# Optimization experiments

Hardware: AMD Instinct MI355X
Metric: run time of the kernel (lower is better)

## Reference

```python
import jax, jax.numpy as jnp
import numpy as np

# ---- static config (matches init_kwargs) ----
B, N_CAMS, C, H, W = 2, 6, 256, 32, 88
BEV_H = BEV_W = 100
NQ = BEV_H * BEV_W
D_PILLAR = 4
HEADS = 8
LEVELS = 3
HEAD_DIM = C // HEADS
PC_RANGE = (-51.2, -51.2, -5.0, 51.2, 51.2, 3.0)
OGFH, OGFW = 256, 704


def _make_lidar2img():
    """Plausible lidar->image projection matrices (K @ [R|t]) for 6 ring cameras."""
    mats = np.zeros((B, N_CAMS, 4, 4), np.float32)
    K = np.array([[557.0, 0.0, OGFW / 2.0], [0.0, 557.0, OGFH / 2.0], [0.0, 0.0, 1.0]], np.float64)
    for b in range(B):
        for n in range(N_CAMS):
            yaw = 2.0 * np.pi * n / N_CAMS + 0.05 * b
            fwd = np.array([np.cos(yaw), np.sin(yaw), 0.0])
            right = np.array([np.sin(yaw), -np.cos(yaw), 0.0])
            down = np.array([0.0, 0.0, -1.0])
            R = np.stack([right, down, fwd])  # lidar -> camera axes
            cam_center = np.array([1.5 * np.cos(yaw), 1.5 * np.sin(yaw), 1.8])
            t = -R @ cam_center
            P = K @ np.concatenate([R, t[:, None]], axis=1)
            mats[b, n, :3, :] = P.astype(np.float32)
            mats[b, n, 3, 3] = 1.0
    return jnp.asarray(mats)


def setup_inputs() -> dict:
    key = jax.random.key(0)
    ks = jax.random.split(key, 16)
    s = 0.02
    return {
        'imgs': jax.random.normal(ks[0], (B, N_CAMS, C, H, W), jnp.float32),
        'lidar2img': _make_lidar2img(),
        'bev_query': jax.random.normal(ks[1], (NQ, 1, C), jnp.float32) * s,
        'bev_pos': jax.random.normal(ks[2], (1, NQ, C), jnp.float32) * s,
        'cams_embeds': jax.random.normal(ks[3], (N_CAMS, C), jnp.float32) * s,
        'level_embeds': jax.random.normal(ks[4], (LEVELS, C), jnp.float32) * s,
        'w_fpn': jax.random.normal(ks[5], (LEVELS, C, C), jnp.float32) * s,
        'b_fpn': jnp.zeros((LEVELS, C), jnp.float32),
        'w_value': jax.random.normal(ks[6], (C, C), jnp.float32) * s,
        'b_value': jnp.zeros((C,), jnp.float32),
        'w_off': jax.random.normal(ks[7], (C, HEADS * LEVELS * D_PILLAR * 2), jnp.float32) * s,
        'b_off': jax.random.normal(ks[8], (HEADS * LEVELS * D_PILLAR * 2,), jnp.float32) * 0.5,
        'w_attn': jax.random.normal(ks[9], (C, HEADS * LEVELS * D_PILLAR), jnp.float32) * s,
        'b_attn': jnp.zeros((HEADS * LEVELS * D_PILLAR,), jnp.float32),
        'w_out': jax.random.normal(ks[10], (C, C), jnp.float32) * s,
        'b_out': jnp.zeros((C,), jnp.float32),
        'w_ts1': jax.random.normal(ks[11], (C, C), jnp.float32) * s,
        'b_ts1': jnp.zeros((C,), jnp.float32),
        'w_ts2': jax.random.normal(ks[12], (C, C), jnp.float32) * s,
        'b_ts2': jnp.zeros((C,), jnp.float32),
    }


def _deform_sample(v, loc, h, w):
    """Bilinear sample (grid_sample, zero padding, align_corners=False).
    v: [N, heads, h*w, dh]; loc: [N, heads, Q, 2] normalized to [0,1]. -> [N, heads, Q, dh]"""
    x = loc[..., 0] * w - 0.5
    y = loc[..., 1] * h - 0.5
    x0 = jnp.floor(x)
    y0 = jnp.floor(y)
    out = jnp.zeros(v.shape[:2] + (loc.shape[2], v.shape[-1]), v.dtype)
    for dx in (0, 1):
        for dy in (0, 1):
            xi = x0 + dx
            yi = y0 + dy
            wgt = (1.0 - jnp.abs(x - xi)) * (1.0 - jnp.abs(y - yi))
            valid = (xi >= 0) & (xi < w) & (yi >= 0) & (yi < h)
            idx = (jnp.clip(yi, 0, h - 1) * w + jnp.clip(xi, 0, w - 1)).astype(jnp.int32)
            g = jnp.take_along_axis(v, idx[..., None], axis=2)
            out = out + g * (wgt * valid)[..., None]
    return out


def _forward(imgs, lidar2img, bev_query, bev_pos, cams_embeds, level_embeds,
             w_fpn, b_fpn, w_value, b_value, w_off, b_off, w_attn, b_attn,
             w_out, b_out, w_ts1, b_ts1, w_ts2, b_ts2):
    # ---- FPN: 3 levels at strides 1/2/4 with per-level 1x1 projection ----
    x = imgs.reshape(B * N_CAMS, C, H, W)
    feats, shapes = [], []
    cur = x
    for l in range(LEVELS):
        if l > 0:
            bn, c, h, w = cur.shape
            cur = cur.reshape(bn, c, h // 2, 2, w // 2, 2).mean(axis=(3, 5))
        f = jnp.einsum('bchw,cd->bdhw', cur, w_fpn[l]) + b_fpn[l][None, :, None, None]
        feats.append(f)
        shapes.append((f.shape[2], f.shape[3]))
    # ---- flatten levels + cam/level embeds: [N, sum_hw, B, C] ----
    flat = []
    for l, f in enumerate(feats):
        h, w = shapes[l]
        fl = jnp.transpose(f.reshape(B, N_CAMS, C, h * w), (1, 0, 3, 2))  # [N,B,hw,C]
        fl = fl + cams_embeds[:, None, None, :] + level_embeds[l][None, None, None, :]
        flat.append(fl)
    feat_flatten = jnp.transpose(jnp.concatenate(flat, axis=2), (0, 2, 1, 3))  # [N,sum_hw,B,C]

    # ---- 3D pillar reference points, normalized [0,1] ----
    zrange = PC_RANGE[5] - PC_RANGE[2]
    zs = jnp.linspace(0.5, zrange - 0.5, D_PILLAR) / zrange
    xs = (jnp.arange(BEV_W, dtype=jnp.float32) + 0.5) / BEV_W
    ys = (jnp.arange(BEV_H, dtype=jnp.float32) + 0.5) / BEV_H
    gy, gx = jnp.meshgrid(ys, xs, indexing='ij')
    ref2d = jnp.stack([gx.ravel(), gy.ravel()], axis=-1)  # [NQ,2]
    ref3d = jnp.concatenate([
        jnp.broadcast_to(ref2d[None], (D_PILLAR, NQ, 2)),
        jnp.broadcast_to(zs[:, None, None].astype(jnp.float32), (D_PILLAR, NQ, 1)),
    ], axis=-1)
    scale = jnp.array([PC_RANGE[3] - PC_RANGE[0], PC_RANGE[4] - PC_RANGE[1], zrange], jnp.float32)
    shift = jnp.array(PC_RANGE[:3], jnp.float32)
    xyz = ref3d * scale + shift
    homog = jnp.concatenate([xyz, jnp.ones((D_PILLAR, NQ, 1), jnp.float32)], axis=-1)

    # ---- point sampling: project to each camera, mask invalid pixels ----
    pts = jnp.einsum('bnij,dqj->nbqdi', lidar2img, homog)  # [N,B,NQ,D,4]
    eps = 1e-5
    depth = pts[..., 2]
    xy = pts[..., :2] / jnp.maximum(depth[..., None], eps)
    ref_cam = xy / jnp.array([OGFW, OGFH], jnp.float32)  # [N,B,NQ,D,2]
    bev_mask = ((depth > eps) & (ref_cam[..., 0] > 0) & (ref_cam[..., 0] < 1)
                & (ref_cam[..., 1] > 0) & (ref_cam[..., 1] < 1))  # [N,B,NQ,D]

    pos = bev_pos[0]  # [NQ,C]

    def sca(query, value, ref_b, mask_b):
        # query [NQ,C]; value [N,sum_hw,C]; ref_b [N,NQ,D,2]; mask_b [N,NQ,D]
        residual = query
        q = query + pos
        v = value @ w_value + b_value
        off = (q @ w_off + b_off).reshape(NQ, HEADS, LEVELS, D_PILLAR, 2)
        attn = jax.nn.softmax((q @ w_attn + b_attn).reshape(NQ, HEADS, LEVELS * D_PILLAR), axis=-1)
        attn = attn.reshape(NQ, HEADS, LEVELS, D_PILLAR)
        out = jnp.zeros((N_CAMS, NQ, HEADS, HEAD_DIM), q.dtype)
        start = 0
        for l, (h, w) in enumerate(shapes):
            hw = h * w
            v_l = jnp.transpose(v[:, start:start + hw].reshape(N_CAMS, hw, HEADS, HEAD_DIM), (0, 2, 1, 3))
            start += hw
            norm = jnp.array([w, h], q.dtype)
            loc = ref_b[:, :, None, :, :] + off[None, :, :, l] / norm  # [N,NQ,heads,D,2]
            loc = jnp.transpose(loc, (0, 2, 1, 3, 4)).reshape(N_CAMS, HEADS, NQ * D_PILLAR, 2)
            s = _deform_sample(v_l, loc, h, w).reshape(N_CAMS, HEADS, NQ, D_PILLAR, HEAD_DIM)
            out = out + jnp.einsum('nhqpd,qhp->nqhd', s, attn[:, :, l])
        out = out.reshape(N_CAMS, NQ, C)
        valid = mask_b.any(axis=-1)  # [N,NQ]
        slots = (out * valid[..., None].astype(out.dtype)).sum(axis=0)
        count = jnp.maximum(valid.sum(axis=0), 1).astype(out.dtype)[:, None]
        slots = slots / count
        return slots @ w_out + b_out + residual

    def tsblock(t):
        return jax.nn.relu(t @ w_ts1 + b_ts1) @ w_ts2 + b_ts2

    bq = jnp.transpose(bev_query, (1, 0, 2))[0]  # [NQ,C]
    groups = []
    ego = bq
    for b in range(B):
        val = feat_flatten[:, :, b, :]
        r = ref_cam[:, b]
        m = bev_mask[:, b]
        if b == 0:
            for _ in range(2):
                bq = tsblock(sca(bq, val, r, m))
            ego = bq
            groups.append(ego.reshape(C, BEV_W, BEV_H))
        else:
            nb = tsblock(sca(ego, val, r, m))
            groups.append(nb.reshape(C, BEV_W, BEV_H))
    bev_groups = jnp.stack(groups, axis=0)  # [B,C,BEV_W,BEV_H]
    return bq[None], bev_groups


def reference(imgs, lidar2img, bev_query, bev_pos, cams_embeds, level_embeds,
              w_fpn, b_fpn, w_value, b_value, w_off, b_off, w_attn, b_attn,
              w_out, b_out, w_ts1, b_ts1, w_ts2, b_ts2):
    return _forward(imgs, lidar2img, bev_query, bev_pos, cams_embeds, level_embeds,
                    w_fpn, b_fpn, w_value, b_value, w_off, b_off, w_attn, b_attn,
                    w_out, b_out, w_ts1, b_ts1, w_ts2, b_ts2)
```

## Files before the change

kernel.cpp:

```cpp
#include <hip/hip_runtime.h>
#include <math.h>

typedef __attribute__((ext_vector_type(8))) short bf16x8;
typedef __attribute__((ext_vector_type(4))) float f32x4;

__device__ __forceinline__ unsigned short f2bf(float x) {
  union { float f; unsigned int u; } v; v.f = x;
  unsigned int r = v.u + 0x7fffu + ((v.u >> 16) & 1u);
  return (unsigned short)(r >> 16);
}
__device__ __forceinline__ float bf2f(unsigned short b) {
  union { unsigned int u; float f; } v; v.u = ((unsigned int)b) << 16; return v.f;
}
__device__ __forceinline__ void split2(float x, unsigned short& h, unsigned short& l) {
  h = f2bf(x);
  l = f2bf(x - bf2f(h));
}
__device__ __forceinline__ int fsi(int q, int c) { return q * 256 + (c ^ ((q & 7) << 2)); }

__device__ __forceinline__ void writeP(unsigned short* __restrict__ P, int col, int k,
                                       unsigned short h, unsigned short l) {
  int tile = col >> 4;
  int lane = (((k >> 3) & 3) << 4) | (col & 15);
  int ks = k >> 5, j8 = k & 7;
  size_t base = ((size_t)(tile >> 1) * 16384) + (size_t)(((tile & 1) << 4) + ks * 2) * 512
              + (size_t)lane * 8 + j8;
  P[base] = h;
  P[base + 512] = l;
}

__device__ __forceinline__ void ld16(const unsigned short* b, bf16x8* f) {
  const unsigned short* b1 = b + 2048;
  const unsigned short* b2 = b + 4096;
  const unsigned short* b3 = b + 6144;
  asm volatile(
    "global_load_dwordx4 %0, %16, off\n\t"
    "global_load_dwordx4 %1, %16, off offset:1024\n\t"
    "global_load_dwordx4 %2, %16, off offset:2048\n\t"
    "global_load_dwordx4 %3, %16, off offset:3072\n\t"
    "global_load_dwordx4 %4, %17, off\n\t"
    "global_load_dwordx4 %5, %17, off offset:1024\n\t"
    "global_load_dwordx4 %6, %17, off offset:2048\n\t"
    "global_load_dwordx4 %7, %17, off offset:3072\n\t"
    "global_load_dwordx4 %8, %18, off\n\t"
    "global_load_dwordx4 %9, %18, off offset:1024\n\t"
    "global_load_dwordx4 %10, %18, off offset:2048\n\t"
    "global_load_dwordx4 %11, %18, off offset:3072\n\t"
    "global_load_dwordx4 %12, %19, off\n\t"
    "global_load_dwordx4 %13, %19, off offset:1024\n\t"
    "global_load_dwordx4 %14, %19, off offset:2048\n\t"
    "global_load_dwordx4 %15, %19, off offset:3072\n\t"
    "s_waitcnt vmcnt(0)"
    : "=&v"(f[0]), "=&v"(f[1]), "=&v"(f[2]), "=&v"(f[3]),
      "=&v"(f[4]), "=&v"(f[5]), "=&v"(f[6]), "=&v"(f[7]),
      "=&v"(f[8]), "=&v"(f[9]), "=&v"(f[10]), "=&v"(f[11]),
      "=&v"(f[12]), "=&v"(f[13]), "=&v"(f[14]), "=&v"(f[15])
    : "v"(b), "v"(b1), "v"(b2), "v"(b3));
}

__device__ __forceinline__ void ld16nw(const unsigned short* b, bf16x8* f) {
  const unsigned short* b1 = b + 2048;
  const unsigned short* b2 = b + 4096;
  const unsigned short* b3 = b + 6144;
  asm volatile(
    "global_load_dwordx4 %0, %16, off\n\t"
    "global_load_dwordx4 %1, %16, off offset:1024\n\t"
    "global_load_dwordx4 %2, %16, off offset:2048\n\t"
    "global_load_dwordx4 %3, %16, off offset:3072\n\t"
    "global_load_dwordx4 %4, %17, off\n\t"
    "global_load_dwordx4 %5, %17, off offset:1024\n\t"
    "global_load_dwordx4 %6, %17, off offset:2048\n\t"
    "global_load_dwordx4 %7, %17, off offset:3072\n\t"
    "global_load_dwordx4 %8, %18, off\n\t"
    "global_load_dwordx4 %9, %18, off offset:1024\n\t"
    "global_load_dwordx4 %10, %18, off offset:2048\n\t"
    "global_load_dwordx4 %11, %18, off offset:3072\n\t"
    "global_load_dwordx4 %12, %19, off\n\t"
    "global_load_dwordx4 %13, %19, off offset:1024\n\t"
    "global_load_dwordx4 %14, %19, off offset:2048\n\t"
    "global_load_dwordx4 %15, %19, off offset:3072"
    : "=&v"(f[0]), "=&v"(f[1]), "=&v"(f[2]), "=&v"(f[3]),
      "=&v"(f[4]), "=&v"(f[5]), "=&v"(f[6]), "=&v"(f[7]),
      "=&v"(f[8]), "=&v"(f[9]), "=&v"(f[10]), "=&v"(f[11]),
      "=&v"(f[12]), "=&v"(f[13]), "=&v"(f[14]), "=&v"(f[15])
    : "v"(b), "v"(b1), "v"(b2), "v"(b3));
}

#define MFMA(a, b, c) __builtin_amdgcn_mfma_f32_16x16x32_bf16(a, b, c, 0, 0, 0)

__device__ __forceinline__ void gemm2t32(
    const unsigned short* __restrict__ Wp, int tile0,
    int lane, int lk, int l15,
    const unsigned short (&AS)[2][32][32][8], f32x4 (&acc)[2][2])
{
  const unsigned short* base = Wp + ((size_t)(tile0 >> 1) * 16384) + (size_t)lane * 8;
  bf16x8 f[32];
  ld16nw(base, f);
  ld16(base + 8192, f + 16);
  __builtin_amdgcn_sched_barrier(0);
#pragma unroll
  for (int ks = 0; ks < 8; ++ks) {
    bf16x8 h0 = f[2 * ks], l0 = f[2 * ks + 1];
    bf16x8 h1 = f[16 + 2 * ks], l1 = f[17 + 2 * ks];
#pragma unroll
    for (int nf = 0; nf < 2; ++nf) {
      bf16x8 bqh = *(const bf16x8*)&AS[0][ks * 4 + lk][nf * 16 + l15][0];
      bf16x8 bql = *(const bf16x8*)&AS[1][ks * 4 + lk][nf * 16 + l15][0];
      acc[0][nf] = MFMA(h0, bqh, acc[0][nf]);
      acc[0][nf] = MFMA(h0, bql, acc[0][nf]);
      acc[0][nf] = MFMA(l0, bqh, acc[0][nf]);
      acc[1][nf] = MFMA(h1, bqh, acc[1][nf]);
      acc[1][nf] = MFMA(h1, bql, acc[1][nf]);
      acc[1][nf] = MFMA(l1, bqh, acc[1][nf]);
    }
  }
}

__device__ __forceinline__ void gemm2t64(
    const unsigned short* __restrict__ Wp, int tile0,
    int lane, int lk, int l15,
    const unsigned short (&AS)[2][32][64][8], f32x4 (&acc)[2][4])
{
  const unsigned short* base = Wp + ((size_t)(tile0 >> 1) * 16384) + (size_t)lane * 8;
  bf16x8 f[32];
  ld16nw(base, f);
  ld16(base + 8192, f + 16);
  __builtin_amdgcn_sched_barrier(0);
#pragma unroll
  for (int ks = 0; ks < 8; ++ks) {
    bf16x8 h0 = f[2 * ks], l0 = f[2 * ks + 1];
    bf16x8 h1 = f[16 + 2 * ks], l1 = f[17 + 2 * ks];
#pragma unroll
    for (int nf = 0; nf < 4; ++nf) {
      bf16x8 bqh = *(const bf16x8*)&AS[0][ks * 4 + lk][nf * 16 + l15][0];
      bf16x8 bql = *(const bf16x8*)&AS[1][ks * 4 + lk][nf * 16 + l15][0];
      acc[0][nf] = MFMA(h0, bqh, acc[0][nf]);
      acc[0][nf] = MFMA(h0, bql, acc[0][nf]);
      acc[0][nf] = MFMA(l0, bqh, acc[0][nf]);
      acc[1][nf] = MFMA(h1, bqh, acc[1][nf]);
      acc[1][nf] = MFMA(h1, bql, acc[1][nf]);
      acc[1][nf] = MFMA(l1, bqh, acc[1][nf]);
    }
  }
}

__device__ __forceinline__ void gemm1t64(
    const unsigned short* __restrict__ Wp, int tile,
    int lane, int lk, int l15,
    const unsigned short (&AS)[2][32][64][8], f32x4 (&acc)[4])
{
  const unsigned short* base = Wp + ((size_t)(tile >> 1) * 16384) + (size_t)(tile & 1) * 8192 + (size_t)lane * 8;
  bf16x8 f[16];
  ld16(base, f);
  __builtin_amdgcn_sched_barrier(0);
#pragma unroll
  for (int ks = 0; ks < 8; ++ks) {
    bf16x8 eh = f[2 * ks], el = f[2 * ks + 1];
#pragma unroll
    for (int nf = 0; nf < 4; ++nf) {
      bf16x8 bqh = *(const bf16x8*)&AS[0][ks * 4 + lk][nf * 16 + l15][0];
      bf16x8 bql = *(const bf16x8*)&AS[1][ks * 4 + lk][nf * 16 + l15][0];
      acc[nf] = MFMA(eh, bqh, acc[nf]);
      acc[nf] = MFMA(eh, bql, acc[nf]);
      acc[nf] = MFMA(el, bqh, acc[nf]);
    }
  }
}

__global__ __launch_bounds__(256) void pool2x2(const float* __restrict__ in, float* __restrict__ out,
                                               int h, int w, int total)
{
  int i = blockIdx.x * 256 + threadIdx.x;
  if (i >= total) return;
  int x = i % w; int r = i / w; int y = r % h; int ci = r / h;
  const float* p = in + (size_t)ci * (4 * h * w) + (size_t)(2 * y) * (2 * w) + 2 * x;
  out[i] = (p[0] + p[1] + p[2 * w] + p[2 * w + 1]) * 0.25f;
}

__global__ __launch_bounds__(256) void prep(
    const float* __restrict__ wo, const float* __restrict__ bo,
    const float* __restrict__ wa, const float* __restrict__ ba,
    const float* __restrict__ wout, const float* __restrict__ wts1, const float* __restrict__ wts2,
    const float* __restrict__ wfpn, const float* __restrict__ wval,
    const float* __restrict__ cams, const float* __restrict__ lev,
    const float* __restrict__ bfpn, const float* __restrict__ bval,
    unsigned short* __restrict__ wcatP, float* __restrict__ bcat,
    unsigned short* __restrict__ woutP, unsigned short* __restrict__ wts1P,
    unsigned short* __restrict__ w45P, unsigned short* __restrict__ wcombP,
    float* __restrict__ e2)
{
  int bb = blockIdx.x, t = threadIdx.x;
  if (bb < 768) {
    int l = bb >> 8, i = bb & 255, j = t;
    const float* a = wfpn + ((size_t)l * 256 + i) * 256;
    float acc = 0.f;
    for (int k = 0; k < 256; ++k) acc = fmaf(a[k], wval[(size_t)k * 256 + j], acc);
    unsigned short h, lo; split2(acc, h, lo);
    writeP(wcombP, l * 256 + j, i, h, lo);
  } else if (bb < 1056) {
    int i = (bb - 768) * 256 + t;
    int c = i >> 8, k = i & 255;
    float v = (c < 192) ? wo[k * 192 + c] : wa[k * 96 + (c - 192)];
    unsigned short h, l; split2(v, h, l);
    writeP(wcatP, c, k, h, l);
    if (i < 288) bcat[i] = (i < 192) ? bo[i] : ba[i - 192];
  } else if (bb < 1312) {
    int i = (bb - 1056) * 256 + t;
    int nn = i >> 8, k = i & 255;
    float v = wout[(size_t)k * 256 + nn];
    unsigned short h, l; split2(v, h, l);
    writeP(woutP, nn, k, h, l);
  } else if (bb < 1568) {
    int i = (bb - 1312) * 256 + t;
    int nn = i >> 8, k = i & 255;
    float v = wts1[(size_t)k * 256 + nn];
    unsigned short h, l; split2(v, h, l);
    writeP(wts1P, nn, k, h, l);
  } else if (bb < 1824) {
    int i = (bb - 1568) * 256 + t;
    int nn = i >> 8, k = i & 255;
    float v = wts2[(size_t)k * 256 + nn];
    unsigned short h, l; split2(v, h, l);
    writeP(w45P, nn, k, h, l);
  } else if (bb < 2112) {
    int mp = bb - 1824;
    int k = t;
    float acc = 0.f;
    for (int j = 0; j < 256; ++j) {
      float wc = (mp < 192) ? wo[j * 192 + mp] : wa[j * 96 + (mp - 192)];
      acc = fmaf(wts2[(size_t)k * 256 + j], wc, acc);
    }
    unsigned short h, l; split2(acc, h, l);
    writeP(w45P, 256 + mp, k, h, l);
  } else {
    int e = bb - 2112;
    int n = e / 3, l = e % 3, j = t;
    float acc = bval[j];
    for (int k = 0; k < 256; ++k) {
      float s = cams[n * 256 + k] + lev[l * 256 + k] + bfpn[l * 256 + k];
      acc = fmaf(s, wval[(size_t)k * 256 + j], acc);
    }
    e2[(size_t)e * 256 + j] = acc;
  }
}

__global__ __launch_bounds__(512) void value_fused(
    const float* __restrict__ imgs, const float* __restrict__ cur1a, const float* __restrict__ cur2a,
    const unsigned short* __restrict__ wcombP,
    const float* __restrict__ e2, float* __restrict__ Vall)
{
  __shared__ __align__(16) unsigned short AS[2][32][32][8];
  int t = threadIdx.x, wid = t >> 6, lane = t & 63, l15 = lane & 15, lk = lane >> 4;
  int bx = blockIdx.x, cam = blockIdx.y, bz = blockIdx.z;
  const float* img0 = imgs + (size_t)bz * 4325376;
  const float* cur1 = cur1a + (size_t)bz * 1081344;
  const float* cur2 = cur2a + (size_t)bz * 270336;
  float* V = Vall + (size_t)bz * 5677056;
  int level, tb, hw; const float* src;
  if (bx < 88)       { level = 0; tb = bx;       hw = 2816; src = img0; }
  else if (bx < 110) { level = 1; tb = bx - 88;  hw = 704;  src = cur1; }
  else               { level = 2; tb = bx - 110; hw = 176;  src = cur2; }
  int p0 = tb * 32;
  const int LST[3] = {0, 2816, 3520};
  src += (size_t)cam * 256 * hw;

  {
    int pos = t & 31, kg = t >> 5;
    bool ok = (p0 + pos) < hw;
    const float* col = src + p0 + pos;
    float vals[16];
#pragma unroll
    for (int i = 0; i < 16; ++i) {
      int k = kg * 16 + i;
      vals[i] = ok ? col[(size_t)k * hw] : 0.f;
    }
#pragma unroll
    for (int half = 0; half < 2; ++half) {
      int ch = kg * 2 + half;
      bf16x8 hv, lv;
#pragma unroll
      for (int j = 0; j < 8; ++j) {
        unsigned short h, l; split2(vals[half * 8 + j], h, l);
        hv[j] = (short)h; lv[j] = (short)l;
      }
      *(bf16x8*)&AS[0][ch][pos][0] = hv;
      *(bf16x8*)&AS[1][ch][pos][0] = lv;
    }
  }
  __syncthreads();

  f32x4 zed = {0.f, 0.f, 0.f, 0.f};
  f32x4 acc[2][2] = {{zed, zed}, {zed, zed}};
  gemm2t32(wcombP, level * 16 + wid * 2, lane, lk, l15, AS, acc);
  __syncthreads();

  float* ASf = (float*)(&AS[0][0][0][0]);
  const float* bias = e2 + (size_t)(cam * 3 + level) * 256;
#pragma unroll
  for (int mf = 0; mf < 2; ++mf) {
    int chb = (wid * 2 + mf) * 16 + lk * 4;
    float4 b4 = *(const float4*)(bias + chb);
#pragma unroll
    for (int nf = 0; nf < 2; ++nf) {
      int q = nf * 16 + l15;
      float4 o;
      o.x = acc[mf][nf][0] + b4.x; o.y = acc[mf][nf][1] + b4.y;
      o.z = acc[mf][nf][2] + b4.z; o.w = acc[mf][nf][3] + b4.w;
      *(float4*)&ASf[fsi(q, chb)] = o;
    }
  }
  __syncthreads();
  float* Vb = V + ((size_t)cam * 3696 + LST[level] + p0) * 256;
#pragma unroll
  for (int j = 0; j < 4; ++j) {
    int g = t + j * 512;
    int q = g >> 6, c = (g & 63) * 4;
    if (p0 + q < hw)
      *(float4*)(Vb + (size_t)q * 256 + c) = *(const float4*)&ASf[fsi(q, c)];
  }
}

__global__ __launch_bounds__(512) void init_fused(
    const float* __restrict__ bev_pos, const float* __restrict__ bev_query,
    const float* __restrict__ bts2,
    const unsigned short* __restrict__ wcatP, const float* __restrict__ bcat,
    float* __restrict__ posA, float* __restrict__ posB,
    float* __restrict__ qtmpA, float* __restrict__ qtmpB)
{
  __shared__ __align__(16) unsigned short AS[2][32][64][8];
  float* ASf = (float*)(&AS[0][0][0][0]);
  int t = threadIdx.x, wid = t >> 6, lane = t & 63, l15 = lane & 15, lk = lane >> 4;
  int r0 = blockIdx.x * 64;
  int y = blockIdx.y;
  const float* base = y ? bev_query : bev_pos;
  const float* padd = y ? bev_pos : nullptr;
  const float* rb = y ? nullptr : bts2;
  float* oA = y ? qtmpA : posA;
  float* oB = y ? qtmpB : posB;
  f32x4 zed = {0.f, 0.f, 0.f, 0.f};

#pragma unroll
  for (int j = 0; j < 8; ++j) {
    int g = t + j * 512;
    int q = g >> 6, c = (g & 63) * 4;
    int rq = r0 + q; if (rq > 9999) rq = 9999;
    float4 a = *(const float4*)(base + (size_t)rq * 256 + c);
    if (padd) {
      float4 p = *(const float4*)(padd + (size_t)rq * 256 + c);
      a.x += p.x; a.y += p.y; a.z += p.z; a.w += p.w;
    }
    if (rb) {
      float4 rv = *(const float4*)(rb + c);
      a.x += rv.x; a.y += rv.y; a.z += rv.z; a.w += rv.w;
    }
    ushort4 hh, ll;
    split2(a.x, hh.x, ll.x); split2(a.y, hh.y, ll.y);
    split2(a.z, hh.z, ll.z); split2(a.w, hh.w, ll.w);
    *(ushort4*)&AS[0][c >> 3][q][c & 7] = hh;
    *(ushort4*)&AS[1][c >> 3][q][c & 7] = ll;
  }
  __syncthreads();

  f32x4 acc[2][4] = {{zed, zed, zed, zed}, {zed, zed, zed, zed}};
  gemm2t64(wcatP, wid * 2, lane, lk, l15, AS, acc);
  f32x4 acc3[4] = {zed, zed, zed, zed};
  if (wid < 2) gemm1t64(wcatP, 16 + wid, lane, lk, l15, AS, acc3);
  __syncthreads();
#pragma unroll
  for (int mf = 0; mf < 2; ++mf) {
    int chb = (wid * 2 + mf) * 16 + lk * 4;
    float4 b4 = *(const float4*)(bcat + chb);
#pragma unroll
    for (int nf = 0; nf < 4; ++nf) {
      int q = nf * 16 + l15;
      float4 o;
      o.x = acc[mf][nf][0] + b4.x; o.y = acc[mf][nf][1] + b4.y;
      o.z = acc[mf][nf][2] + b4.z; o.w = acc[mf][nf][3] + b4.w;
      *(float4*)&ASf[fsi(q, chb)] = o;
    }
  }
  if (wid < 2) {
    int ce = wid * 16 + lk * 4;
    float4 b4 = *(const float4*)(bcat + 256 + ce);
#pragma unroll
    for (int nf = 0; nf < 4; ++nf) {
      int qg = r0 + nf * 16 + l15;
      if (qg < 10000) {
        float4 o;
        o.x = acc3[nf][0] + b4.x; o.y = acc3[nf][1] + b4.y;
        o.z = acc3[nf][2] + b4.z; o.w = acc3[nf][3] + b4.w;
        *(float4*)(oB + (size_t)qg * 32 + ce) = o;
      }
    }
  }
  __syncthreads();
#pragma unroll
  for (int j = 0; j < 8; ++j) {
    int g = t + j * 512;
    int q = g >> 6, c = (g & 63) * 4;
    int qg = r0 + q;
    if (qg < 10000)
      *(float4*)(oA + (size_t)qg * 256 + c) = *(const float4*)&ASf[fsi(q, c)];
  }
}

__global__ __launch_bounds__(512) void fused_iter(
    const float* __restrict__ slots, const float* __restrict__ qin,
    const unsigned short* __restrict__ woutP, const unsigned short* __restrict__ wts1P,
    const unsigned short* __restrict__ w45P,
    const float* __restrict__ bout, const float* __restrict__ bts1,
    const float* __restrict__ bts2,
    float* __restrict__ qout, float* __restrict__ outA, float* __restrict__ outB,
    float* __restrict__ qtmpA, float* __restrict__ qtmpB)
{
  __shared__ __align__(16) unsigned short AS[2][32][64][8];
  float* ASf = (float*)(&AS[0][0][0][0]);
  int t = threadIdx.x, wid = t >> 6, lane = t & 63, l15 = lane & 15, lk = lane >> 4;
  int r0 = blockIdx.x * 64;
  f32x4 zed = {0.f, 0.f, 0.f, 0.f};

#pragma unroll
  for (int j = 0; j < 8; ++j) {
    int g = t + j * 512;
    int q = g >> 6, c = (g & 63) * 4;
    int rq = r0 + q; if (rq > 9999) rq = 9999;
    float4 a = *(const float4*)(slots + (size_t)rq * 256 + c);
    ushort4 hh, ll;
    split2(a.x, hh.x, ll.x); split2(a.y, hh.y, ll.y);
    split2(a.z, hh.z, ll.z); split2(a.w, hh.w, ll.w);
    *(ushort4*)&AS[0][c >> 3][q][c & 7] = hh;
    *(ushort4*)&AS[1][c >> 3][q][c & 7] = ll;
  }
  __syncthreads();

  {
    f32x4 acc[2][4] = {{zed, zed, zed, zed}, {zed, zed, zed, zed}};
    gemm2t64(woutP, wid * 2, lane, lk, l15, AS, acc);
    __syncthreads();
    float4 qreg[8];
#pragma unroll
    for (int j = 0; j < 8; ++j) {
      int g = t + j * 512;
      int q = g >> 6, c = (g & 63) * 4;
      int rq = r0 + q; if (rq > 9999) rq = 9999;
      qreg[j] = *(const float4*)(qin + (size_t)rq * 256 + c);
    }
#pragma unroll
    for (int j = 0; j < 8; ++j) {
      int g = t + j * 512;
      int q = g >> 6, c = (g & 63) * 4;
      *(float4*)&ASf[fsi(q, c)] = qreg[j];
    }
    __syncthreads();
    float4 rr[2][4];
#pragma unroll
    for (int mf = 0; mf < 2; ++mf) {
      int chb = (wid * 2 + mf) * 16 + lk * 4;
#pragma unroll
      for (int nf = 0; nf < 4; ++nf)
        rr[mf][nf] = *(const float4*)&ASf[fsi(nf * 16 + l15, chb)];
    }
    __syncthreads();
#pragma unroll
    for (int mf = 0; mf < 2; ++mf) {
      int chb = (wid * 2 + mf) * 16 + lk * 4;
      float4 b4 = *(const float4*)(bout + chb);
#pragma unroll
      for (int nf = 0; nf < 4; ++nf) {
        int q = nf * 16 + l15;
        float v0 = acc[mf][nf][0] + b4.x + rr[mf][nf].x;
        float v1 = acc[mf][nf][1] + b4.y + rr[mf][nf].y;
        float v2 = acc[mf][nf][2] + b4.z + rr[mf][nf].z;
        float v3 = acc[mf][nf][3] + b4.w + rr[mf][nf].w;
        ushort4 hh, ll;
        split2(v0, hh.x, ll.x); split2(v1, hh.y, ll.y);
        split2(v2, hh.z, ll.z); split2(v3, hh.w, ll.w);
        *(ushort4*)&AS[0][chb >> 3][q][chb & 7] = hh;
        *(ushort4*)&AS[1][chb >> 3][q][chb & 7] = ll;
      }
    }
    __syncthreads();
  }
  {
    f32x4 acc[2][4] = {{zed, zed, zed, zed}, {zed, zed, zed, zed}};
    gemm2t64(wts1P, wid * 2, lane, lk, l15, AS, acc);
    __syncthreads();
#pragma unroll
    for (int mf = 0; mf < 2; ++mf) {
      int chb = (wid * 2 + mf) * 16 + lk * 4;
      float4 b4 = *(const float4*)(bts1 + chb);
#pragma unroll
      for (int nf = 0; nf < 4; ++nf) {
        int q = nf * 16 + l15;
        float v0 = fmaxf(acc[mf][nf][0] + b4.x, 0.f);
        float v1 = fmaxf(acc[mf][nf][1] + b4.y, 0.f);
        float v2 = fmaxf(acc[mf][nf][2] + b4.z, 0.f);
        float v3 = fmaxf(acc[mf][nf][3] + b4.w, 0.f);
        ushort4 hh, ll;
        split2(v0, hh.x, ll.x); split2(v1, hh.y, ll.y);
        split2(v2, hh.z, ll.z); split2(v3, hh.w, ll.w);
        *(ushort4*)&AS[0][chb >> 3][q][chb & 7] = hh;
        *(ushort4*)&AS[1][chb >> 3][q][chb & 7] = ll;
      }
    }
    __syncthreads();
  }
  {
    f32x4 accA[2][4] = {{zed, zed, zed, zed}, {zed, zed, zed, zed}};
    f32x4 accB[2][4] = {{zed, zed, zed, zed}, {zed, zed, zed, zed}};
    if (wid < 4 || qtmpA) {
      gemm2t64(w45P, wid * 4,     lane, lk, l15, AS, accA);
      gemm2t64(w45P, wid * 4 + 2, lane, lk, l15, AS, accB);
    }
    f32x4 acc3[4] = {zed, zed, zed, zed};
    if (qtmpA && wid < 2) gemm1t64(w45P, 32 + wid, lane, lk, l15, AS, acc3);
    __syncthreads();
    if (wid < 4) {
#pragma unroll
      for (int half = 0; half < 2; ++half) {
#pragma unroll
        for (int mf = 0; mf < 2; ++mf) {
          int chb = (wid * 4 + half * 2 + mf) * 16 + lk * 4;
          float4 b4 = *(const float4*)(bts2 + chb);
#pragma unroll
          for (int nf = 0; nf < 4; ++nf) {
            int q = nf * 16 + l15;
            f32x4 a = half ? accB[mf][nf] : accA[mf][nf];
            float4 o;
            o.x = a[0] + b4.x; o.y = a[1] + b4.y;
            o.z = a[2] + b4.z; o.w = a[3] + b4.w;
            *(float4*)&ASf[fsi(q, chb)] = o;
          }
        }
      }
    }
    if (qtmpA && wid < 2) {
      int ce = wid * 16 + lk * 4;
#pragma unroll
      for (int nf = 0; nf < 4; ++nf) {
        int qg = r0 + nf * 16 + l15;
        if (qg < 10000) {
          float4 o;
          o.x = acc3[nf][0]; o.y = acc3[nf][1]; o.z = acc3[nf][2]; o.w = acc3[nf][3];
          *(float4*)(qtmpB + (size_t)qg * 32 + ce) = o;
        }
      }
    }
    __syncthreads();
#pragma unroll
    for (int j = 0; j < 8; ++j) {
      int g = t + j * 512;
      int q = g >> 6, c = (g & 63) * 4;
      int qg = r0 + q;
      if (qg < 10000) {
        float4 vq = *(const float4*)&ASf[fsi(q, c)];
        size_t go = (size_t)qg * 256 + c;
        *(float4*)(qout + go) = vq;
        if (outA) { *(float4*)(outA + go) = vq; *(float4*)(outB + go) = vq; }
      }
    }
    if (!qtmpA) return;
    __syncthreads();
    if (wid >= 4) {
#pragma unroll
      for (int half = 0; half < 2; ++half) {
#pragma unroll
        for (int mf = 0; mf < 2; ++mf) {
          int cc = ((wid - 4) * 4 + half * 2 + mf) * 16 + lk * 4;
#pragma unroll
          for (int nf = 0; nf < 4; ++nf) {
            int q = nf * 16 + l15;
            f32x4 a = half ? accB[mf][nf] : accA[mf][nf];
            float4 o;
            o.x = a[0]; o.y = a[1]; o.z = a[2]; o.w = a[3];
            *(float4*)&ASf[fsi(q, cc)] = o;
          }
        }
      }
    }
    __syncthreads();
#pragma unroll
    for (int j = 0; j < 8; ++j) {
      int g = t + j * 512;
      int q = g >> 6, c = (g & 63) * 4;
      int qg = r0 + q;
      if (qg < 10000)
        *(float4*)(qtmpA + (size_t)qg * 256 + c) = *(const float4*)&ASf[fsi(q, c)];
    }
  }
}

__global__ __launch_bounds__(256) void sca_sample(const float* __restrict__ qtmpA, const float* __restrict__ qtmpB,
                                                  const float* __restrict__ posA, const float* __restrict__ posB,
                                                  const float* __restrict__ V,
                                                  const float* __restrict__ l2i, float* __restrict__ slots)
{
  int b = blockIdx.x;
  int q = (b & 7) * 1250 + (b >> 3);
  int t = threadIdx.x;
  int head = t >> 5;
  __shared__ float raw[288];
  __shared__ float attnS[96];
  __shared__ float refx[6][4], refy[6][4];
  __shared__ int mnd[24];
  __shared__ int validn[6];
  __shared__ __align__(16) float w4[576][4];
  __shared__ __align__(16) int o4[576][4];

  {
    float x = qtmpA[(size_t)q * 256 + t];
    if (posA) x += posA[(size_t)q * 256 + t];
    raw[t] = x;
    if (t < 32) {
      float y = qtmpB[(size_t)q * 32 + t];
      if (posB) y += posB[(size_t)q * 32 + t];
      raw[256 + t] = y;
    }
  }
  if (t >= 32 && t < 56) {
    int tt = t - 32;
    int n = tt >> 2, d = tt & 3;
    const float* Mrow = l2i + n * 16;
    int qx = q % 100, qy = q / 100;
    float X = ((qx + 0.5f) / 100.0f) * 102.4f + (-51.2f);
    float Y = ((qy + 0.5f) / 100.0f) * 102.4f + (-51.2f);
    float zi = (d == 3) ? 7.5f : (0.5f + (float)d * (7.0f / 3.0f));
    float Z = zi + (-5.0f);
    float px = Mrow[0] * X + Mrow[1] * Y + Mrow[2] * Z + Mrow[3];
    float py = Mrow[4] * X + Mrow[5] * Y + Mrow[6] * Z + Mrow[7];
    float pz = Mrow[8] * X + Mrow[9] * Y + Mrow[10] * Z + Mrow[11];
    float dz = fmaxf(pz, 1e-5f);
    float xc = (px / dz) / 704.0f;
    float yc = (py / dz) / 256.0f;
    refx[n][d] = xc; refy[n][d] = yc;
    mnd[n * 4 + d] = (pz > 1e-5f) && (xc > 0.f) && (xc < 1.f) && (yc > 0.f) && (yc < 1.f);
  }
  __syncthreads();
  if (t < 8) {
    float mx = raw[192 + t * 12];
    for (int p = 1; p < 12; ++p) mx = fmaxf(mx, raw[192 + t * 12 + p]);
    float s = 0.f;
    float e[12];
#pragma unroll
    for (int p = 0; p < 12; ++p) { e[p] = __expf(raw[192 + t * 12 + p] - mx); s += e[p]; }
    float inv = 1.f / s;
#pragma unroll
    for (int p = 0; p < 12; ++p) attnS[t * 12 + p] = e[p] * inv;
  } else if (t < 14) {
    int n = t - 8;
    validn[n] = mnd[n * 4] | mnd[n * 4 + 1] | mnd[n * 4 + 2] | mnd[n * 4 + 3];
  }
  __syncthreads();

  int packed = 0, nv = 0;
#pragma unroll
  for (int n = 0; n < 6; ++n)
    if (validn[n]) { packed |= n << (3 * nv); nv++; }
  float invc = 1.f / (float)(nv > 1 ? nv : 1);

  const float WWf[3] = {88.f, 44.f, 22.f}, HHf[3] = {32.f, 16.f, 8.f};
  const int WWi[3] = {88, 44, 22}, STi[3] = {0, 2816, 3520};
  int npts = nv * 96;
  for (int pt = t; pt < npts; pt += 256) {
    int hd = pt & 7;
    int g = pt >> 3;
    int j = g % 12, ni = g / 12;
    int n = (packed >> (3 * ni)) & 7;
    int l = j >> 2, d = j & 3;
    float wwf = WWf[l], hhf = HHf[l];
    int wwi = WWi[l], st = STi[l];
    float a = attnS[hd * 12 + j] * invc;
    float ox = raw[hd * 24 + l * 8 + d * 2 + 0];
    float oy = raw[hd * 24 + l * 8 + d * 2 + 1];
    float x = refx[n][d] * wwf + ox - 0.5f;
    float y = refy[n][d] * hhf + oy - 0.5f;
    float x0 = floorf(x), y0 = floorf(y);
    float fx = x - x0, fy = y - y0;
    float wx0 = 1.f - fx, wy0 = 1.f - fy;
    float vx0 = (x0 >= 0.f && x0 < wwf) ? 1.f : 0.f;
    float vx1 = (x0 + 1.f >= 0.f && x0 + 1.f < wwf) ? 1.f : 0.f;
    float vy0 = (y0 >= 0.f && y0 < hhf) ? 1.f : 0.f;
    float vy1 = (y0 + 1.f >= 0.f && y0 + 1.f < hhf) ? 1.f : 0.f;
    w4[pt][0] = a * wx0 * wy0 * vx0 * vy0;
    w4[pt][1] = a * fx * wy0 * vx1 * vy0;
    w4[pt][2] = a * wx0 * fy * vx0 * vy1;
    w4[pt][3] = a * fx * fy * vx1 * vy1;
    int ix0 = (int)fminf(fmaxf(x0, 0.f), wwf - 1.f);
    int ix1 = (int)fminf(fmaxf(x0 + 1.f, 0.f), wwf - 1.f);
    int iy0 = (int)fminf(fmaxf(y0, 0.f), hhf - 1.f);
    int iy1 = (int)fminf(fmaxf(y0 + 1.f, 0.f), hhf - 1.f);
    int rA = (st + iy0 * wwi) << 10, rB = (st + iy1 * wwi) << 10;
    o4[pt][0] = rA + (ix0 << 10);
    o4[pt][1] = rA + (ix1 << 10);
    o4[pt][2] = rB + (ix0 << 10);
    o4[pt][3] = rB + (ix1 << 10);
  }
  __syncthreads();

  int t4 = t << 2;
  float acc0 = 0.f, acc1 = 0.f;
  int sl = 0;
#pragma unroll
  for (int n = 0; n < 6; ++n) {
    if (!validn[n]) continue;
    const char* Vn = (const char*)(V + (size_t)n * 946176);
    int pb = sl * 96 + head;
    sl++;
    float va[48];
#pragma unroll
    for (int j = 0; j < 12; ++j) {
      int4 o = *reinterpret_cast<const int4*>(&o4[pb + j * 8][0]);
      va[4 * j + 0] = *(const float*)(Vn + (unsigned)(o.x + t4));
      va[4 * j + 1] = *(const float*)(Vn + (unsigned)(o.y + t4));
      va[4 * j + 2] = *(const float*)(Vn + (unsigned)(o.z + t4));
      va[4 * j + 3] = *(const float*)(Vn + (unsigned)(o.w + t4));
    }
#pragma unroll
    for (int j = 0; j < 12; ++j) {
      float4 w = *reinterpret_cast<const float4*>(&w4[pb + j * 8][0]);
      acc0 = fmaf(w.x, va[4 * j + 0], acc0);
      acc1 = fmaf(w.y, va[4 * j + 1], acc1);
      acc0 = fmaf(w.z, va[4 * j + 2], acc0);
      acc1 = fmaf(w.w, va[4 * j + 3], acc1);
    }
  }
  slots[(size_t)q * 256 + t] = acc0 + acc1;
}

extern "C" void kernel_launch(void* const* d_in, const int* in_sizes, int n_in,
                              void* d_out, int out_size, void* d_ws, size_t ws_size,
                              hipStream_t stream)
{
  const float* imgs = (const float*)d_in[0];
  const float* l2i = (const float*)d_in[1];
  const float* bev_query = (const float*)d_in[2];
  const float* bev_pos = (const float*)d_in[3];
  const float* cams = (const float*)d_in[4];
  const float* lev = (const float*)d_in[5];
  const float* wfpn = (const float*)d_in[6];
  const float* bfpn = (const float*)d_in[7];
  const float* wval = (const float*)d_in[8];
  const float* bval = (const float*)d_in[9];
  const float* woff = (const float*)d_in[10];
  const float* boff = (const float*)d_in[11];
  const float* wattn = (const float*)d_in[12];
  const float* battn = (const float*)d_in[13];
  const float* wout = (const float*)d_in[14];
  const float* bout = (const float*)d_in[15];
  const float* wts1 = (const float*)d_in[16];
  const float* bts1 = (const float*)d_in[17];
  const float* wts2 = (const float*)d_in[18];
  const float* bts2 = (const float*)d_in[19];

  float* W = (float*)d_ws;
  size_t off = 0;
  auto alloc = [&](size_t n) { float* p = W + off; off += n; return p; };
  float* v    = alloc((size_t)2 * 5677056);
  float* cur1 = alloc((size_t)12 * 256 * 16 * 44);
  float* cur2 = alloc((size_t)12 * 256 * 8 * 22);
  float* bqA  = alloc(2560000);
  float* bqB  = alloc(2560000);
  float* qtmpA = alloc(2560000);
  float* qtmpB = alloc(320000);
  float* posA = alloc(2560000);
  float* posB = alloc(320000);
  float* slots = alloc(2560000);
  float* wcombPR = alloc(196608);
  float* wcatPR = alloc(73728);
  float* woutPR = alloc(65536);
  float* wts1PR = alloc(65536);
  float* w45PR = alloc(139264);
  float* bcat = alloc(512);
  float* e2 = alloc(4608);
  (void)ws_size; (void)in_sizes; (void)n_in; (void)out_size;

  unsigned short* wcombP = (unsigned short*)wcombPR;
  unsigned short* wcatP = (unsigned short*)wcatPR;
  unsigned short* woutP = (unsigned short*)woutPR;
  unsigned short* wts1P = (unsigned short*)wts1PR;
  unsigned short* w45P = (unsigned short*)w45PR;

  float* v0 = v;
  float* v1 = v + 5677056;
  float* OUT = (float*)d_out;

  pool2x2<<<8448, 256, 0, stream>>>(imgs, cur1, 16, 44, 2162688);
  pool2x2<<<2112, 256, 0, stream>>>(cur1, cur2, 8, 22, 540672);
  prep<<<2130, 256, 0, stream>>>(woff, boff, wattn, battn, wout, wts1, wts2, wfpn, wval,
                                 cams, lev, bfpn, bval,
                                 wcatP, bcat, woutP, wts1P, w45P, wcombP, e2);

  init_fused<<<dim3(157, 2), 512, 0, stream>>>(bev_pos, bev_query, bts2, wcatP, bcat,
                                               posA, posB, qtmpA, qtmpB);

  value_fused<<<dim3(116, 6, 2), 512, 0, stream>>>(imgs, cur1, cur2, wcombP, e2, v);

  sca_sample<<<10000, 256, 0, stream>>>(qtmpA, qtmpB, nullptr, nullptr, v0, l2i, slots);
  fused_iter<<<157, 512, 0, stream>>>(slots, bev_query,
      woutP, wts1P, w45P, bout, bts1, bts2,
      bqA, nullptr, nullptr, qtmpA, qtmpB);
  sca_sample<<<10000, 256, 0, stream>>>(qtmpA, qtmpB, posA, posB, v0, l2i, slots);
  fused_iter<<<157, 512, 0, stream>>>(slots, bqA,
      woutP, wts1P, w45P, bout, bts1, bts2,
      bqB, OUT, OUT + 2560000, qtmpA, qtmpB);
  sca_sample<<<10000, 256, 0, stream>>>(qtmpA, qtmpB, posA, posB, v1, l2i + 96, slots);
  fused_iter<<<157, 512, 0, stream>>>(slots, bqB,
      woutP, wts1P, w45P, bout, bts1, bts2,
      OUT + 5120000, nullptr, nullptr, nullptr, nullptr);
}
```

Before: 283.1 us.

## Merge pooling with prep and value projection with init into combined launches

The first 2x2 pooling is folded into the weight-prep kernel as extra blocks, and the value projection and BEV query init GEMMs are merged into one launch using blockIdx.z to pick the role. The value projection tile grows from 32 to 64 positions per block so it can reuse the 64-wide GEMM path, halving its block count. This removes two kernel launches and lets independent work run at the same time, at the cost of more registers per thread (32 loaded values) and some idle blocks in the third z-slice.

```diff
diff --git a/kernel.cpp b/kernel.cpp
--- a/kernel.cpp
+++ b/kernel.cpp
@@ -88,34 +88,6 @@
 
 #define MFMA(a, b, c) __builtin_amdgcn_mfma_f32_16x16x32_bf16(a, b, c, 0, 0, 0)
 
-__device__ __forceinline__ void gemm2t32(
-    const unsigned short* __restrict__ Wp, int tile0,
-    int lane, int lk, int l15,
-    const unsigned short (&AS)[2][32][32][8], f32x4 (&acc)[2][2])
-{
-  const unsigned short* base = Wp + ((size_t)(tile0 >> 1) * 16384) + (size_t)lane * 8;
-  bf16x8 f[32];
-  ld16nw(base, f);
-  ld16(base + 8192, f + 16);
-  __builtin_amdgcn_sched_barrier(0);
-#pragma unroll
-  for (int ks = 0; ks < 8; ++ks) {
-    bf16x8 h0 = f[2 * ks], l0 = f[2 * ks + 1];
-    bf16x8 h1 = f[16 + 2 * ks], l1 = f[17 + 2 * ks];
-#pragma unroll
-    for (int nf = 0; nf < 2; ++nf) {
-      bf16x8 bqh = *(const bf16x8*)&AS[0][ks * 4 + lk][nf * 16 + l15][0];
-      bf16x8 bql = *(const bf16x8*)&AS[1][ks * 4 + lk][nf * 16 + l15][0];
-      acc[0][nf] = MFMA(h0, bqh, acc[0][nf]);
-      acc[0][nf] = MFMA(h0, bql, acc[0][nf]);
-      acc[0][nf] = MFMA(l0, bqh, acc[0][nf]);
-      acc[1][nf] = MFMA(h1, bqh, acc[1][nf]);
-      acc[1][nf] = MFMA(h1, bql, acc[1][nf]);
-      acc[1][nf] = MFMA(l1, bqh, acc[1][nf]);
-    }
-  }
-}
-
 __device__ __forceinline__ void gemm2t64(
     const unsigned short* __restrict__ Wp, int tile0,
     int lane, int lk, int l15,
@@ -177,7 +149,8 @@
   out[i] = (p[0] + p[1] + p[2 * w] + p[2 * w + 1]) * 0.25f;
 }
 
-__global__ __launch_bounds__(256) void prep(
+__global__ __launch_bounds__(256) void pp(
+    const float* __restrict__ imgs, float* __restrict__ cur1,
     const float* __restrict__ wo, const float* __restrict__ bo,
     const float* __restrict__ wa, const float* __restrict__ ba,
     const float* __restrict__ wout, const float* __restrict__ wts1, const float* __restrict__ wts2,
@@ -189,7 +162,17 @@
     unsigned short* __restrict__ w45P, unsigned short* __restrict__ wcombP,
     float* __restrict__ e2)
 {
-  int bb = blockIdx.x, t = threadIdx.x;
+  int blk = blockIdx.x, t = threadIdx.x;
+  if (blk < 8448) {
+    int i = blk * 256 + t;
+    if (i >= 2162688) return;
+    const int h = 16, w = 44;
+    int x = i % w; int r = i / w; int y = r % h; int ci = r / h;
+    const float* p = imgs + (size_t)ci * (4 * h * w) + (size_t)(2 * y) * (2 * w) + 2 * x;
+    cur1[i] = (p[0] + p[1] + p[2 * w] + p[2 * w + 1]) * 0.25f;
+    return;
+  }
+  int bb = blk - 8448;
   if (bb < 768) {
     int l = bb >> 8, i = bb & 255, j = t;
     const float* a = wfpn + ((size_t)l * 256 + i) * 256;
@@ -244,83 +227,10 @@
   }
 }
 
-__global__ __launch_bounds__(512) void value_fused(
+__global__ __launch_bounds__(512) void vi_fused(
     const float* __restrict__ imgs, const float* __restrict__ cur1a, const float* __restrict__ cur2a,
-    const unsigned short* __restrict__ wcombP,
-    const float* __restrict__ e2, float* __restrict__ Vall)
-{
-  __shared__ __align__(16) unsigned short AS[2][32][32][8];
-  int t = threadIdx.x, wid = t >> 6, lane = t & 63, l15 = lane & 15, lk = lane >> 4;
-  int bx = blockIdx.x, cam = blockIdx.y, bz = blockIdx.z;
-  const float* img0 = imgs + (size_t)bz * 4325376;
-  const float* cur1 = cur1a + (size_t)bz * 1081344;
-  const float* cur2 = cur2a + (size_t)bz * 270336;
-  float* V = Vall + (size_t)bz * 5677056;
-  int level, tb, hw; const float* src;
-  if (bx < 88)       { level = 0; tb = bx;       hw = 2816; src = img0; }
-  else if (bx < 110) { level = 1; tb = bx - 88;  hw = 704;  src = cur1; }
-  else               { level = 2; tb = bx - 110; hw = 176;  src = cur2; }
-  int p0 = tb * 32;
-  const int LST[3] = {0, 2816, 3520};
-  src += (size_t)cam * 256 * hw;
-
-  {
-    int pos = t & 31, kg = t >> 5;
-    bool ok = (p0 + pos) < hw;
-    const float* col = src + p0 + pos;
-    float vals[16];
-#pragma unroll
-    for (int i = 0; i < 16; ++i) {
-      int k = kg * 16 + i;
-      vals[i] = ok ? col[(size_t)k * hw] : 0.f;
-    }
-#pragma unroll
-    for (int half = 0; half < 2; ++half) {
-      int ch = kg * 2 + half;
-      bf16x8 hv, lv;
-#pragma unroll
-      for (int j = 0; j < 8; ++j) {
-        unsigned short h, l; split2(vals[half * 8 + j], h, l);
-        hv[j] = (short)h; lv[j] = (short)l;
-      }
-      *(bf16x8*)&AS[0][ch][pos][0] = hv;
-      *(bf16x8*)&AS[1][ch][pos][0] = lv;
-    }
-  }
-  __syncthreads();
-
-  f32x4 zed = {0.f, 0.f, 0.f, 0.f};
-  f32x4 acc[2][2] = {{zed, zed}, {zed, zed}};
-  gemm2t32(wcombP, level * 16 + wid * 2, lane, lk, l15, AS, acc);
-  __syncthreads();
-
-  float* ASf = (float*)(&AS[0][0][0][0]);
-  const float* bias = e2 + (size_t)(cam * 3 + level) * 256;
-#pragma unroll
-  for (int mf = 0; mf < 2; ++mf) {
-    int chb = (wid * 2 + mf) * 16 + lk * 4;
-    float4 b4 = *(const float4*)(bias + chb);
-#pragma unroll
-    for (int nf = 0; nf < 2; ++nf) {
-      int q = nf * 16 + l15;
-      float4 o;
-      o.x = acc[mf][nf][0] + b4.x; o.y = acc[mf][nf][1] + b4.y;
-      o.z = acc[mf][nf][2] + b4.z; o.w = acc[mf][nf][3] + b4.w;
-      *(float4*)&ASf[fsi(q, chb)] = o;
-    }
-  }
-  __syncthreads();
-  float* Vb = V + ((size_t)cam * 3696 + LST[level] + p0) * 256;
-#pragma unroll
-  for (int j = 0; j < 4; ++j) {
-    int g = t + j * 512;
-    int q = g >> 6, c = (g & 63) * 4;
-    if (p0 + q < hw)
-      *(float4*)(Vb + (size_t)q * 256 + c) = *(const float4*)&ASf[fsi(q, c)];
-  }
-}
-
-__global__ __launch_bounds__(512) void init_fused(
+    const unsigned short* __restrict__ wcombP, const float* __restrict__ e2,
+    float* __restrict__ Vall,
     const float* __restrict__ bev_pos, const float* __restrict__ bev_query,
     const float* __restrict__ bts2,
     const unsigned short* __restrict__ wcatP, const float* __restrict__ bcat,
@@ -330,77 +240,151 @@
   __shared__ __align__(16) unsigned short AS[2][32][64][8];
   float* ASf = (float*)(&AS[0][0][0][0]);
   int t = threadIdx.x, wid = t >> 6, lane = t & 63, l15 = lane & 15, lk = lane >> 4;
-  int r0 = blockIdx.x * 64;
-  int y = blockIdx.y;
-  const float* base = y ? bev_query : bev_pos;
-  const float* padd = y ? bev_pos : nullptr;
-  const float* rb = y ? nullptr : bts2;
-  float* oA = y ? qtmpA : posA;
-  float* oB = y ? qtmpB : posB;
   f32x4 zed = {0.f, 0.f, 0.f, 0.f};
 
-#pragma unroll
-  for (int j = 0; j < 8; ++j) {
-    int g = t + j * 512;
-    int q = g >> 6, c = (g & 63) * 4;
-    int rq = r0 + q; if (rq > 9999) rq = 9999;
-    float4 a = *(const float4*)(base + (size_t)rq * 256 + c);
-    if (padd) {
-      float4 p = *(const float4*)(padd + (size_t)rq * 256 + c);
-      a.x += p.x; a.y += p.y; a.z += p.z; a.w += p.w;
-    }
-    if (rb) {
-      float4 rv = *(const float4*)(rb + c);
-      a.x += rv.x; a.y += rv.y; a.z += rv.z; a.w += rv.w;
-    }
-    ushort4 hh, ll;
-    split2(a.x, hh.x, ll.x); split2(a.y, hh.y, ll.y);
-    split2(a.z, hh.z, ll.z); split2(a.w, hh.w, ll.w);
-    *(ushort4*)&AS[0][c >> 3][q][c & 7] = hh;
-    *(ushort4*)&AS[1][c >> 3][q][c & 7] = ll;
-  }
-  __syncthreads();
-
-  f32x4 acc[2][4] = {{zed, zed, zed, zed}, {zed, zed, zed, zed}};
-  gemm2t64(wcatP, wid * 2, lane, lk, l15, AS, acc);
-  f32x4 acc3[4] = {zed, zed, zed, zed};
-  if (wid < 2) gemm1t64(wcatP, 16 + wid, lane, lk, l15, AS, acc3);
-  __syncthreads();
-#pragma unroll
-  for (int mf = 0; mf < 2; ++mf) {
-    int chb = (wid * 2 + mf) * 16 + lk * 4;
-    float4 b4 = *(const float4*)(bcat + chb);
-#pragma unroll
-    for (int nf = 0; nf < 4; ++nf) {
-      int q = nf * 16 + l15;
-      float4 o;
-      o.x = acc[mf][nf][0] + b4.x; o.y = acc[mf][nf][1] + b4.y;
-      o.z = acc[mf][nf][2] + b4.z; o.w = acc[mf][nf][3] + b4.w;
-      *(float4*)&ASf[fsi(q, chb)] = o;
-    }
-  }
-  if (wid < 2) {
-    int ce = wid * 16 + lk * 4;
-    float4 b4 = *(const float4*)(bcat + 256 + ce);
-#pragma unroll
-    for (int nf = 0; nf < 4; ++nf) {
-      int qg = r0 + nf * 16 + l15;
-      if (qg < 10000) {
+  if (blockIdx.z < 2) {
+    int bx = blockIdx.x, cam = blockIdx.y, bz = blockIdx.z;
+    const float* img0 = imgs + (size_t)bz * 4325376;
+    const float* cur1 = cur1a + (size_t)bz * 1081344;
+    const float* cur2 = cur2a + (size_t)bz * 270336;
+    float* V = Vall + (size_t)bz * 5677056;
+    int level, tb, hw; const float* src;
+    if (bx < 44)      { level = 0; tb = bx;      hw = 2816; src = img0; }
+    else if (bx < 55) { level = 1; tb = bx - 44; hw = 704;  src = cur1; }
+    else              { level = 2; tb = bx - 55; hw = 176;  src = cur2; }
+    int p0 = tb * 64;
+    const int LST[3] = {0, 2816, 3520};
+    src += (size_t)cam * 256 * hw;
+
+    {
+      int pos = t & 63, kg = t >> 6;
+      bool ok = (p0 + pos) < hw;
+      const float* col = src + p0 + pos;
+      float vals[32];
+#pragma unroll
+      for (int i = 0; i < 32; ++i) {
+        int k = kg * 32 + i;
+        vals[i] = ok ? col[(size_t)k * hw] : 0.f;
+      }
+#pragma unroll
+      for (int qt = 0; qt < 4; ++qt) {
+        int ch = kg * 4 + qt;
+        bf16x8 hv, lv;
+#pragma unroll
+        for (int j = 0; j < 8; ++j) {
+          unsigned short h, l; split2(vals[qt * 8 + j], h, l);
+          hv[j] = (short)h; lv[j] = (short)l;
+        }
+        *(bf16x8*)&AS[0][ch][pos][0] = hv;
+        *(bf16x8*)&AS[1][ch][pos][0] = lv;
+      }
+    }
+    __syncthreads();
+
+    f32x4 acc[2][4] = {{zed, zed, zed, zed}, {zed, zed, zed, zed}};
+    gemm2t64(wcombP, level * 16 + wid * 2, lane, lk, l15, AS, acc);
+    __syncthreads();
+
+    const float* bias = e2 + (size_t)(cam * 3 + level) * 256;
+#pragma unroll
+    for (int mf = 0; mf < 2; ++mf) {
+      int chb = (wid * 2 + mf) * 16 + lk * 4;
+      float4 b4 = *(const float4*)(bias + chb);
+#pragma unroll
+      for (int nf = 0; nf < 4; ++nf) {
+        int q = nf * 16 + l15;
         float4 o;
-        o.x = acc3[nf][0] + b4.x; o.y = acc3[nf][1] + b4.y;
-        o.z = acc3[nf][2] + b4.z; o.w = acc3[nf][3] + b4.w;
-        *(float4*)(oB + (size_t)qg * 32 + ce) = o;
-      }
-    }
-  }
-  __syncthreads();
-#pragma unroll
-  for (int j = 0; j < 8; ++j) {
-    int g = t + j * 512;
-    int q = g >> 6, c = (g & 63) * 4;
-    int qg = r0 + q;
-    if (qg < 10000)
-      *(float4*)(oA + (size_t)qg * 256 + c) = *(const float4*)&ASf[fsi(q, c)];
+        o.x = acc[mf][nf][0] + b4.x; o.y = acc[mf][nf][1] + b4.y;
+        o.z = acc[mf][nf][2] + b4.z; o.w = acc[mf][nf][3] + b4.w;
+        *(float4*)&ASf[fsi(q, chb)] = o;
+      }
+    }
+    __syncthreads();
+    float* Vb = V + ((size_t)cam * 3696 + LST[level] + p0) * 256;
+#pragma unroll
+    for (int j = 0; j < 8; ++j) {
+      int g = t + j * 512;
+      int q = g >> 6, c = (g & 63) * 4;
+      if (p0 + q < hw)
+        *(float4*)(Vb + (size_t)q * 256 + c) = *(const float4*)&ASf[fsi(q, c)];
+    }
+    return;
+  }
+
+  {
+    int id = blockIdx.y * 58 + blockIdx.x;
+    if (id >= 314) return;
+    int r0 = (id >> 1) * 64;
+    int y = id & 1;
+    const float* base = y ? bev_query : bev_pos;
+    const float* padd = y ? bev_pos : nullptr;
+    const float* rb = y ? nullptr : bts2;
+    float* oA = y ? qtmpA : posA;
+    float* oB = y ? qtmpB : posB;
+
+#pragma unroll
+    for (int j = 0; j < 8; ++j) {
+      int g = t + j * 512;
+      int q = g >> 6, c = (g & 63) * 4;
+      int rq = r0 + q; if (rq > 9999) rq = 9999;
+      float4 a = *(const float4*)(base + (size_t)rq * 256 + c);
+      if (padd) {
+        float4 p = *(const float4*)(padd + (size_t)rq * 256 + c);
+        a.x += p.x; a.y += p.y; a.z += p.z; a.w += p.w;
+      }
+      if (rb) {
+        float4 rv = *(const float4*)(rb + c);
+        a.x += rv.x; a.y += rv.y; a.z += rv.z; a.w += rv.w;
+      }
+      ushort4 hh, ll;
+      split2(a.x, hh.x, ll.x); split2(a.y, hh.y, ll.y);
+      split2(a.z, hh.z, ll.z); split2(a.w, hh.w, ll.w);
+      *(ushort4*)&AS[0][c >> 3][q][c & 7] = hh;
+      *(ushort4*)&AS[1][c >> 3][q][c & 7] = ll;
+    }
+    __syncthreads();
+
+    f32x4 acc[2][4] = {{zed, zed, zed, zed}, {zed, zed, zed, zed}};
+    gemm2t64(wcatP, wid * 2, lane, lk, l15, AS, acc);
+    f32x4 acc3[4] = {zed, zed, zed, zed};
+    if (wid < 2) gemm1t64(wcatP, 16 + wid, lane, lk, l15, AS, acc3);
+    __syncthreads();
+#pragma unroll
+    for (int mf = 0; mf < 2; ++mf) {
+      int chb = (wid * 2 + mf) * 16 + lk * 4;
+      float4 b4 = *(const float4*)(bcat + chb);
+#pragma unroll
+      for (int nf = 0; nf < 4; ++nf) {
+        int q = nf * 16 + l15;
+        float4 o;
+        o.x = acc[mf][nf][0] + b4.x; o.y = acc[mf][nf][1] + b4.y;
+        o.z = acc[mf][nf][2] + b4.z; o.w = acc[mf][nf][3] + b4.w;
+        *(float4*)&ASf[fsi(q, chb)] = o;
+      }
+    }
+    if (wid < 2) {
+      int ce = wid * 16 + lk * 4;
+      float4 b4 = *(const float4*)(bcat + 256 + ce);
+#pragma unroll
+      for (int nf = 0; nf < 4; ++nf) {
+        int qg = r0 + nf * 16 + l15;
+        if (qg < 10000) {
+          float4 o;
+          o.x = acc3[nf][0] + b4.x; o.y = acc3[nf][1] + b4.y;
+          o.z = acc3[nf][2] + b4.z; o.w = acc3[nf][3] + b4.w;
+          *(float4*)(oB + (size_t)qg * 32 + ce) = o;
+        }
+      }
+    }
+    __syncthreads();
+#pragma unroll
+    for (int j = 0; j < 8; ++j) {
+      int g = t + j * 512;
+      int q = g >> 6, c = (g & 63) * 4;
+      int qg = r0 + q;
+      if (qg < 10000)
+        *(float4*)(oA + (size_t)qg * 256 + c) = *(const float4*)&ASf[fsi(q, c)];
+    }
   }
 }
 
@@ -784,16 +768,15 @@
   float* v1 = v + 5677056;
   float* OUT = (float*)d_out;
 
-  pool2x2<<<8448, 256, 0, stream>>>(imgs, cur1, 16, 44, 2162688);
+  pp<<<8448 + 2130, 256, 0, stream>>>(imgs, cur1,
+                                      woff, boff, wattn, battn, wout, wts1, wts2, wfpn, wval,
+                                      cams, lev, bfpn, bval,
+                                      wcatP, bcat, woutP, wts1P, w45P, wcombP, e2);
   pool2x2<<<2112, 256, 0, stream>>>(cur1, cur2, 8, 22, 540672);
-  prep<<<2130, 256, 0, stream>>>(woff, boff, wattn, battn, wout, wts1, wts2, wfpn, wval,
-                                 cams, lev, bfpn, bval,
-                                 wcatP, bcat, woutP, wts1P, w45P, wcombP, e2);
-
-  init_fused<<<dim3(157, 2), 512, 0, stream>>>(bev_pos, bev_query, bts2, wcatP, bcat,
+
+  vi_fused<<<dim3(58, 6, 3), 512, 0, stream>>>(imgs, cur1, cur2, wcombP, e2, v,
+                                               bev_pos, bev_query, bts2, wcatP, bcat,
                                                posA, posB, qtmpA, qtmpB);
-
-  value_fused<<<dim3(116, 6, 2), 512, 0, stream>>>(imgs, cur1, cur2, wcombP, e2, v);
 
   sca_sample<<<10000, 256, 0, stream>>>(qtmpA, qtmpB, nullptr, nullptr, v0, l2i, slots);
   fused_iter<<<157, 512, 0, stream>>>(slots, bev_query,
```

New measurement: 295.8 us. 4.5% more time.
